# Kernel tuning notes

Hardware: AMD Instinct MI355X
Metric: run time of the kernel (lower is better)

The kernel has to match this reference:

```python
import jax, jax.numpy as jnp
import numpy as np

# Model dims (match init_kwargs)
B, S, H = 1, 2048, 1024
E = 16            # n_routed_experts
I = 768           # moe_intermediate_size
TOPK = 4          # num_experts_per_tok
G = 4             # n_group
TOPK_G = 2        # topk_group
SCALE = 2.5       # routed_scaling_factor
N_SHARED = 1      # n_shared_experts


def setup_inputs() -> dict:
    key = jax.random.key(0)
    ks = jax.random.split(key, 9)
    def rn(k, shape, scale=0.02):
        return jax.random.normal(k, shape, dtype=jnp.float32) * scale
    return dict(
        hidden_states=jax.random.normal(ks[0], (B, S, H), dtype=jnp.float32),
        gate_w=rn(ks[1], (E, H)),
        gate_bias=jax.random.normal(ks[2], (E,), dtype=jnp.float32) * 0.1,
        w1=rn(ks[3], (E, I, H)),   # gate_proj weights [out,in]
        w2=rn(ks[4], (E, H, I)),   # down_proj weights
        w3=rn(ks[5], (E, I, H)),   # up_proj weights
        ws1=rn(ks[6], (I * N_SHARED, H)),
        ws2=rn(ks[7], (H, I * N_SHARED)),
        ws3=rn(ks[8], (I * N_SHARED, H)),
    )


def _route(x, gate_w, gate_bias):
    """noaux_tc routing: sigmoid scores + bias, group top-k, top_k experts."""
    n = x.shape[0]
    logits = jnp.einsum('nh,eh->ne', x.astype(jnp.float32), gate_w)  # [N,E]
    scores = jax.nn.sigmoid(logits)
    sb = scores + gate_bias                                          # biased scores
    # group score = sum of top-2 biased scores in each group
    gs = sb.reshape(n, G, E // G)
    group_scores = jnp.sum(jax.lax.top_k(gs, 2)[0], axis=-1)         # [N,G]
    _, gidx = jax.lax.top_k(group_scores, TOPK_G)                    # [N,TOPK_G]
    gmask = jnp.sum(jax.nn.one_hot(gidx, G, dtype=sb.dtype), axis=1) # [N,G]
    emask = jnp.repeat(gmask, E // G, axis=-1)                       # [N,E]
    masked = jnp.where(emask > 0, sb, -jnp.inf)
    _, tidx = jax.lax.top_k(masked, TOPK)                            # [N,TOPK]
    w = jnp.take_along_axis(scores, tidx, axis=1)                    # unbiased weights
    w = w / (jnp.sum(w, axis=-1, keepdims=True) + 1e-20)             # norm_topk_prob
    return tidx, w * SCALE


def reference(hidden_states, gate_w, gate_bias, w1, w2, w3, ws1, ws2, ws3):
    b, s, h = hidden_states.shape
    x = hidden_states.reshape(-1, h)                                 # [N,H]
    tidx, tw = _route(x, gate_w, gate_bias)
    n = x.shape[0]
    # dense combine weights [N,E] (zero for unselected experts)
    combine = jnp.zeros((n, E), x.dtype).at[jnp.arange(n)[:, None], tidx].add(tw)
    # grouped SwiGLU experts (dense-over-experts reference form)
    g = jnp.einsum('nh,eih->nei', x, w1)
    u = jnp.einsum('nh,eih->nei', x, w3)
    hact = jax.nn.silu(g) * u * combine[:, :, None]
    y = jnp.einsum('nei,ehi->nh', hact, w2)
    # shared expert SwiGLU
    shared = jnp.einsum('ni,hi->nh', jax.nn.silu(x @ ws1.T) * (x @ ws3.T), ws2)
    return (y + shared).reshape(b, s, h)
```

## Files before the change

### kernel.cpp

```cpp
#include <hip/hip_runtime.h>
#include <hip/hip_bf16.h>
#include <math.h>

#define N_TOK 2048
#define H_DIM 1024
#define N_EXP 16
#define I_DIM 768
#define TOPK 4
#define SCALE 2.5f
#define MAX_TILES 96

typedef __attribute__((ext_vector_type(8))) short bf16x8;
typedef __attribute__((ext_vector_type(4))) float f32x4;

#define OFF_COUNTS   0
#define OFF_OFFSETS  128
#define OFF_TILES    256
#define OFF_TOKIDS   768
#define OFF_TOKW     (OFF_TOKIDS + N_EXP*N_TOK*4)
#define OFF_XB       (OFF_TOKW + N_EXP*N_TOK*4)
#define OFF_HACT     (OFF_XB + (size_t)N_TOK*H_DIM*2)
#define OFF_WB1      (OFF_HACT + (size_t)N_TOK*(TOPK+1)*I_DIM*2)
#define OFF_WB2      (OFF_WB1 + (size_t)N_EXP*I_DIM*H_DIM*2)
#define OFF_WB3      (OFF_WB2 + (size_t)N_EXP*H_DIM*I_DIM*2)
#define OFF_WSB1     (OFF_WB3 + (size_t)N_EXP*I_DIM*H_DIM*2)
#define OFF_WSB2     (OFF_WSB1 + (size_t)I_DIM*H_DIM*2)
#define OFF_WSB3     (OFF_WSB2 + (size_t)H_DIM*I_DIM*2)
#define OFF_GWT      (OFF_WSB3 + (size_t)I_DIM*H_DIM*2)

__device__ __forceinline__ ushort f2bf(float f) {
    union { __hip_bfloat16 h; ushort u; } cv;
    cv.h = __float2bfloat16(f);
    return cv.u;
}
__device__ __forceinline__ unsigned pack2(float lo, float hi) {
    return (unsigned)f2bf(lo) | ((unsigned)f2bf(hi) << 16);
}
__device__ __forceinline__ void async_copy16(const void* g, void* l) {
    __builtin_amdgcn_global_load_lds(
        (const __attribute__((address_space(1))) unsigned int*)g,
        (__attribute__((address_space(3))) unsigned int*)l, 16, 0, 0);
}

struct WcArgs {
    const float* src[7];
    ushort* dst[7];
    int n4[7];
};
__global__ void k_wconv(WcArgs a) {
    int id = blockIdx.y;
    const float4* s = (const float4*)a.src[id];
    uint2* d = (uint2*)a.dst[id];
    int n4 = a.n4[id];
    int stride = gridDim.x * 256;
    for (int i = blockIdx.x * 256 + threadIdx.x; i < n4; i += stride) {
        float4 v = s[i];
        uint2 p;
        p.x = pack2(v.x, v.y);
        p.y = pack2(v.z, v.w);
        d[i] = p;
    }
}

__global__ void k_gwt(const float* __restrict__ gw, float* __restrict__ gwT) {
    int i = blockIdx.x * 256 + threadIdx.x;
    int k = i >> 4, e = i & 15;
    gwT[i] = gw[e * H_DIM + k];
}

__launch_bounds__(256)
__global__ void k_route(const float* __restrict__ x, const float* __restrict__ gwT,
                        const float* __restrict__ gb,
                        int* __restrict__ counts, int* __restrict__ tok_ids,
                        float* __restrict__ tok_w) {
    __shared__ float lgs[4][N_EXP + 1];
    int tid = threadIdx.x;
    int wv = tid >> 6, lane = tid & 63;
    int e = lane & 15, ks = lane >> 4;
    int n = blockIdx.x * 4 + wv;

    const float* xr = x + (size_t)n * H_DIM + ks * 256;
    const float* wr = gwT + ks * 256 * N_EXP + e;
    float a0 = 0.f, a1 = 0.f, a2 = 0.f, a3 = 0.f;
#pragma unroll 8
    for (int k = 0; k < 256; k += 4) {
        float4 xv = *(const float4*)(xr + k);
        a0 += xv.x * wr[(k + 0) * N_EXP];
        a1 += xv.y * wr[(k + 1) * N_EXP];
        a2 += xv.z * wr[(k + 2) * N_EXP];
        a3 += xv.w * wr[(k + 3) * N_EXP];
    }
    float acc = (a0 + a1) + (a2 + a3);
    acc += __shfl_xor(acc, 16);
    acc += __shfl_xor(acc, 32);
    if (lane < 16) lgs[wv][lane] = acc;
    __syncthreads();

    if (tid < 4) {
        int n2 = blockIdx.x * 4 + tid;
        float sc[N_EXP], sb[N_EXP];
        for (int ee = 0; ee < N_EXP; ee++) {
            float l = lgs[tid][ee];
            sc[ee] = 1.f / (1.f + expf(-l));
            sb[ee] = sc[ee] + gb[ee];
        }
        float gsc[4];
        for (int g = 0; g < 4; g++) {
            float m1 = -1e30f, m2 = -1e30f;
            for (int j = 0; j < 4; j++) {
                float v = sb[4 * g + j];
                if (v > m1) { m2 = m1; m1 = v; }
                else if (v > m2) m2 = v;
            }
            gsc[g] = m1 + m2;
        }
        int g1 = 0;
        for (int g = 1; g < 4; g++) if (gsc[g] > gsc[g1]) g1 = g;
        int g2 = -1;
        for (int g = 0; g < 4; g++) {
            if (g == g1) continue;
            if (g2 < 0 || gsc[g] > gsc[g2]) g2 = g;
        }
        bool allowed[N_EXP];
        for (int ee = 0; ee < N_EXP; ee++) {
            int grp = ee >> 2;
            allowed[ee] = (grp == g1) || (grp == g2);
        }
        int chosen[TOPK];
        float wsum = 0.f;
        for (int k = 0; k < TOPK; k++) {
            int best = -1;
            for (int ee = 0; ee < N_EXP; ee++) {
                if (!allowed[ee]) continue;
                if (best < 0 || sb[ee] > sb[best]) best = ee;
            }
            chosen[k] = best;
            allowed[best] = false;
            wsum += sc[best];
        }
        float inv = SCALE / (wsum + 1e-20f);
        for (int k = 0; k < TOPK; k++) {
            int ee = chosen[k];
            int p = atomicAdd(&counts[ee], 1);
            tok_ids[ee * N_TOK + p] = n2;
            tok_w[ee * N_TOK + p] = sc[ee] * inv;
        }
    }
}

__global__ void k_scan(const int* __restrict__ counts, int* __restrict__ offsets,
                       int* __restrict__ tiles) {
    if (threadIdx.x == 0 && blockIdx.x == 0) {
        int off = 0;
        for (int e = 0; e < N_EXP; e++) { offsets[e] = off; off += counts[e]; }
        offsets[N_EXP] = off;
        int t = 0;
        for (int e = 0; e < N_EXP; e++)
            for (int m0 = 0; m0 < counts[e]; m0 += 128)
                tiles[t++] = e | ((m0 >> 7) << 5);
        for (int m0 = 0; m0 < N_TOK; m0 += 128)
            tiles[t++] = N_EXP | ((m0 >> 7) << 5);
        for (; t < MAX_TILES; t++) tiles[t] = -1;
    }
}

__launch_bounds__(256, 4)
__global__ void k_gateup(const ushort* __restrict__ xb, const ushort* __restrict__ wb1,
                         const ushort* __restrict__ wb3, const ushort* __restrict__ wsb1,
                         const ushort* __restrict__ wsb3, const int* __restrict__ counts,
                         const int* __restrict__ offsets, const int* __restrict__ tiles,
                         const int* __restrict__ tok_ids, const float* __restrict__ tok_w,
                         ushort* __restrict__ hact) {
    int desc = tiles[blockIdx.x];
    if (desc < 0) return;
    int e = desc & 31;
    int m0 = (desc >> 5) * 128;
    int i0 = blockIdx.y * 64;
    int Me = (e == N_EXP) ? N_TOK : counts[e];
    const ushort* W1 = (e == N_EXP) ? wsb1 : wb1 + (size_t)e * I_DIM * H_DIM;
    const ushort* W3 = (e == N_EXP) ? wsb3 : wb3 + (size_t)e * I_DIM * H_DIM;
    int base = offsets[e];

    __shared__ ushort As[128][64];
    __shared__ ushort Bs[128][64];
    __shared__ float tws[128];

    int tid = threadIdx.x;
    int wv = tid >> 6, lane = tid & 63;
    int seg = lane & 7, rsub = lane >> 3;
    int gch = (seg ^ rsub) * 8;

    if (tid < 128) {
        int r = m0 + tid;
        tws[tid] = (e == N_EXP) ? 1.f : ((r < Me) ? tok_w[e * N_TOK + r] : 0.f);
    }

    const ushort* aptr[4];
#pragma unroll
    for (int j = 0; j < 4; j++) {
        int gr = m0 + wv * 32 + j * 8 + rsub;
        int tok = (e == N_EXP) ? gr : ((gr < Me) ? tok_ids[e * N_TOK + gr] : 0);
        aptr[j] = xb + (size_t)tok * H_DIM + gch;
    }
    const ushort* bptr[4];
#pragma unroll
    for (int j = 0; j < 4; j++) {
        int r = wv * 32 + j * 8 + rsub;
        const ushort* W = (r < 64) ? (W1 + (size_t)(i0 + r) * H_DIM)
                                   : (W3 + (size_t)(i0 + r - 64) * H_DIM);
        bptr[j] = W + gch;
    }

    int quad = lane >> 4, lr = lane & 15, rx = lr & 7;
    f32x4 acc[2][8] = {};

    const int NK = H_DIM / 64;
    for (int k = 0; k < NK; k++) {
        int off = k * 64;
#pragma unroll
        for (int j = 0; j < 4; j++) async_copy16(aptr[j] + off, &As[wv * 32 + j * 8][0]);
#pragma unroll
        for (int j = 0; j < 4; j++) async_copy16(bptr[j] + off, &Bs[wv * 32 + j * 8][0]);
        __syncthreads();
#pragma unroll
        for (int ks = 0; ks < 2; ks++) {
            int co = ((ks * 4 + quad) ^ rx) * 8;
            bf16x8 a0 = *(const bf16x8*)&As[wv * 32 + lr][co];
            bf16x8 a1 = *(const bf16x8*)&As[wv * 32 + 16 + lr][co];
#pragma unroll
            for (int ni = 0; ni < 8; ni++) {
                bf16x8 bf = *(const bf16x8*)&Bs[ni * 16 + lr][co];
                acc[0][ni] = __builtin_amdgcn_mfma_f32_16x16x32_bf16(a0, bf, acc[0][ni], 0, 0, 0);
                acc[1][ni] = __builtin_amdgcn_mfma_f32_16x16x32_bf16(a1, bf, acc[1][ni], 0, 0, 0);
            }
        }
        __syncthreads();
    }

#pragma unroll
    for (int mi = 0; mi < 2; mi++) {
#pragma unroll
        for (int ni = 0; ni < 4; ni++) {
            f32x4 g = acc[mi][ni];
            f32x4 u = acc[mi][ni + 4];
#pragma unroll
            for (int rg = 0; rg < 4; rg++) {
                int ml = wv * 32 + mi * 16 + quad * 4 + rg;
                int row = m0 + ml;
                if (row < Me) {
                    float gg = g[rg], uu = u[rg];
                    float act = (gg / (1.f + expf(-gg))) * uu * tws[ml];
                    hact[(size_t)(base + row) * I_DIM + i0 + ni * 16 + lr] = f2bf(act);
                }
            }
        }
    }
}

__launch_bounds__(256, 4)
__global__ void k_down(const ushort* __restrict__ hact, const ushort* __restrict__ wb2,
                       const ushort* __restrict__ wsb2, const int* __restrict__ counts,
                       const int* __restrict__ offsets, const int* __restrict__ tiles,
                       const int* __restrict__ tok_ids, float* __restrict__ out) {
    int desc = tiles[blockIdx.x];
    if (desc < 0) return;
    int e = desc & 31;
    int m0 = (desc >> 5) * 128;
    int h0 = blockIdx.y * 128;
    int Me = (e == N_EXP) ? N_TOK : counts[e];
    const ushort* W2 = (e == N_EXP) ? wsb2 : wb2 + (size_t)e * H_DIM * I_DIM;
    int base = offsets[e];

    __shared__ ushort As[128][64];
    __shared__ ushort Bs[128][64];
    __shared__ int toks[128];

    int tid = threadIdx.x;
    int wv = tid >> 6, lane = tid & 63;
    int seg = lane & 7, rsub = lane >> 3;
    int gch = (seg ^ rsub) * 8;

    if (tid < 128) {
        int r = m0 + tid;
        toks[tid] = (e == N_EXP) ? r : ((r < Me) ? tok_ids[e * N_TOK + r] : 0);
    }

    const ushort* aptr[4];
#pragma unroll
    for (int j = 0; j < 4; j++) {
        int row = wv * 32 + j * 8 + rsub;
        aptr[j] = hact + (size_t)(base + m0 + row) * I_DIM + gch;
    }
    const ushort* bptr[4];
#pragma unroll
    for (int j = 0; j < 4; j++) {
        int r = wv * 32 + j * 8 + rsub;
        bptr[j] = W2 + (size_t)(h0 + r) * I_DIM + gch;
    }

    int quad = lane >> 4, lr = lane & 15, rx = lr & 7;
    f32x4 acc[2][8] = {};

    const int NK = I_DIM / 64;
    for (int k = 0; k < NK; k++) {
        int off = k * 64;
#pragma unroll
        for (int j = 0; j < 4; j++) async_copy16(aptr[j] + off, &As[wv * 32 + j * 8][0]);
#pragma unroll
        for (int j = 0; j < 4; j++) async_copy16(bptr[j] + off, &Bs[wv * 32 + j * 8][0]);
        __syncthreads();
#pragma unroll
        for (int ks = 0; ks < 2; ks++) {
            int co = ((ks * 4 + quad) ^ rx) * 8;
            bf16x8 a0 = *(const bf16x8*)&As[wv * 32 + lr][co];
            bf16x8 a1 = *(const bf16x8*)&As[wv * 32 + 16 + lr][co];
#pragma unroll
            for (int ni = 0; ni < 8; ni++) {
                bf16x8 bf = *(const bf16x8*)&Bs[ni * 16 + lr][co];
                acc[0][ni] = __builtin_amdgcn_mfma_f32_16x16x32_bf16(a0, bf, acc[0][ni], 0, 0, 0);
                acc[1][ni] = __builtin_amdgcn_mfma_f32_16x16x32_bf16(a1, bf, acc[1][ni], 0, 0, 0);
            }
        }
        __syncthreads();
    }

#pragma unroll
    for (int mi = 0; mi < 2; mi++) {
#pragma unroll
        for (int ni = 0; ni < 8; ni++) {
#pragma unroll
            for (int rg = 0; rg < 4; rg++) {
                int ml = wv * 32 + mi * 16 + quad * 4 + rg;
                int row = m0 + ml;
                if (row < Me) {
                    int tok = toks[ml];
                    atomicAdd(&out[(size_t)tok * H_DIM + h0 + ni * 16 + lr],
                              acc[mi][ni][rg]);
                }
            }
        }
    }
}

extern "C" void kernel_launch(void* const* d_in, const int* in_sizes, int n_in,
                              void* d_out, int out_size, void* d_ws, size_t ws_size,
                              hipStream_t stream) {
    const float* x   = (const float*)d_in[0];
    const float* gw  = (const float*)d_in[1];
    const float* gb  = (const float*)d_in[2];
    const float* w1  = (const float*)d_in[3];
    const float* w2  = (const float*)d_in[4];
    const float* w3  = (const float*)d_in[5];
    const float* ws1 = (const float*)d_in[6];
    const float* ws2 = (const float*)d_in[7];
    const float* ws3 = (const float*)d_in[8];
    float* out = (float*)d_out;

    char* wsb = (char*)d_ws;
    int* counts   = (int*)(wsb + OFF_COUNTS);
    int* offsets  = (int*)(wsb + OFF_OFFSETS);
    int* tiles    = (int*)(wsb + OFF_TILES);
    int* tok_ids  = (int*)(wsb + OFF_TOKIDS);
    float* tok_w  = (float*)(wsb + OFF_TOKW);
    ushort* xb    = (ushort*)(wsb + OFF_XB);
    ushort* hact  = (ushort*)(wsb + OFF_HACT);
    ushort* wb1   = (ushort*)(wsb + OFF_WB1);
    ushort* wb2   = (ushort*)(wsb + OFF_WB2);
    ushort* wb3   = (ushort*)(wsb + OFF_WB3);
    ushort* wsb1  = (ushort*)(wsb + OFF_WSB1);
    ushort* wsb2  = (ushort*)(wsb + OFF_WSB2);
    ushort* wsb3  = (ushort*)(wsb + OFF_WSB3);
    float* gwT    = (float*)(wsb + OFF_GWT);

    hipMemsetAsync(wsb, 0, 128, stream);
    hipMemsetAsync(d_out, 0, (size_t)out_size * 4, stream);

    WcArgs wa;
    wa.src[0] = w1;  wa.dst[0] = wb1;  wa.n4[0] = N_EXP * I_DIM * H_DIM / 4;
    wa.src[1] = w2;  wa.dst[1] = wb2;  wa.n4[1] = N_EXP * H_DIM * I_DIM / 4;
    wa.src[2] = w3;  wa.dst[2] = wb3;  wa.n4[2] = N_EXP * I_DIM * H_DIM / 4;
    wa.src[3] = ws1; wa.dst[3] = wsb1; wa.n4[3] = I_DIM * H_DIM / 4;
    wa.src[4] = ws2; wa.dst[4] = wsb2; wa.n4[4] = H_DIM * I_DIM / 4;
    wa.src[5] = ws3; wa.dst[5] = wsb3; wa.n4[5] = I_DIM * H_DIM / 4;
    wa.src[6] = x;   wa.dst[6] = xb;   wa.n4[6] = N_TOK * H_DIM / 4;
    k_wconv<<<dim3(3072, 7), 256, 0, stream>>>(wa);

    k_gwt<<<N_EXP * H_DIM / 256, 256, 0, stream>>>(gw, gwT);
    k_route<<<N_TOK / 4, 256, 0, stream>>>(x, gwT, gb, counts, tok_ids, tok_w);
    k_scan<<<1, 1, 0, stream>>>(counts, offsets, tiles);
    {
        dim3 grid(MAX_TILES, I_DIM / 64);
        k_gateup<<<grid, 256, 0, stream>>>(xb, wb1, wb3, wsb1, wsb3, counts, offsets,
                                           tiles, tok_ids, tok_w, hact);
    }
    {
        dim3 grid(MAX_TILES, H_DIM / 128);
        k_down<<<grid, 256, 0, stream>>>(hact, wb2, wsb2, counts, offsets, tiles,
                                         tok_ids, out);
    }
}
```

Measured before the change: 363.5 us.

## Fuse fp32-to-bf16 weight conversion into expert GEMM tile loads

Removes the separate pass that converted all expert and shared weights to bf16. The gate/up and down GEMM kernels now read fp32 weights directly, register-prefetch the next K slice, and pack to bf16 while storing into the swizzled LDS tile. Only the activations get a small dedicated conversion kernel. This avoids a full read and write of every weight each call, but the GEMMs now fetch twice as many bytes per weight tile, once for each token tile, and do the B staging through registers rather than async LDS copies.

```diff
diff --git a/kernel.cpp b/kernel.cpp
--- a/kernel.cpp
+++ b/kernel.cpp
@@ -20,13 +20,7 @@
 #define OFF_TOKW     (OFF_TOKIDS + N_EXP*N_TOK*4)
 #define OFF_XB       (OFF_TOKW + N_EXP*N_TOK*4)
 #define OFF_HACT     (OFF_XB + (size_t)N_TOK*H_DIM*2)
-#define OFF_WB1      (OFF_HACT + (size_t)N_TOK*(TOPK+1)*I_DIM*2)
-#define OFF_WB2      (OFF_WB1 + (size_t)N_EXP*I_DIM*H_DIM*2)
-#define OFF_WB3      (OFF_WB2 + (size_t)N_EXP*H_DIM*I_DIM*2)
-#define OFF_WSB1     (OFF_WB3 + (size_t)N_EXP*I_DIM*H_DIM*2)
-#define OFF_WSB2     (OFF_WSB1 + (size_t)I_DIM*H_DIM*2)
-#define OFF_WSB3     (OFF_WSB2 + (size_t)H_DIM*I_DIM*2)
-#define OFF_GWT      (OFF_WSB3 + (size_t)I_DIM*H_DIM*2)
+#define OFF_GWT      (OFF_HACT + (size_t)N_TOK*(TOPK+1)*I_DIM*2)
 
 __device__ __forceinline__ ushort f2bf(float f) {
     union { __hip_bfloat16 h; ushort u; } cv;
@@ -41,25 +35,18 @@
         (const __attribute__((address_space(1))) unsigned int*)g,
         (__attribute__((address_space(3))) unsigned int*)l, 16, 0, 0);
 }
-
-struct WcArgs {
-    const float* src[7];
-    ushort* dst[7];
-    int n4[7];
-};
-__global__ void k_wconv(WcArgs a) {
-    int id = blockIdx.y;
-    const float4* s = (const float4*)a.src[id];
-    uint2* d = (uint2*)a.dst[id];
-    int n4 = a.n4[id];
-    int stride = gridDim.x * 256;
-    for (int i = blockIdx.x * 256 + threadIdx.x; i < n4; i += stride) {
-        float4 v = s[i];
-        uint2 p;
-        p.x = pack2(v.x, v.y);
-        p.y = pack2(v.z, v.w);
-        d[i] = p;
-    }
+__device__ __forceinline__ uint4 pack8(float4 a, float4 b) {
+    uint4 p;
+    p.x = pack2(a.x, a.y); p.y = pack2(a.z, a.w);
+    p.z = pack2(b.x, b.y); p.w = pack2(b.z, b.w);
+    return p;
+}
+
+__global__ void k_xconv(const float* __restrict__ x, ushort* __restrict__ xb) {
+    int idx = (blockIdx.x * 256 + threadIdx.x) * 8;
+    float4 a = *(const float4*)(x + idx);
+    float4 b = *(const float4*)(x + idx + 4);
+    *(uint4*)(xb + idx) = pack8(a, b);
 }
 
 __global__ void k_gwt(const float* __restrict__ gw, float* __restrict__ gwT) {
@@ -165,9 +152,9 @@
 }
 
 __launch_bounds__(256, 4)
-__global__ void k_gateup(const ushort* __restrict__ xb, const ushort* __restrict__ wb1,
-                         const ushort* __restrict__ wb3, const ushort* __restrict__ wsb1,
-                         const ushort* __restrict__ wsb3, const int* __restrict__ counts,
+__global__ void k_gateup(const ushort* __restrict__ xb, const float* __restrict__ w1,
+                         const float* __restrict__ w3, const float* __restrict__ ws1,
+                         const float* __restrict__ ws3, const int* __restrict__ counts,
                          const int* __restrict__ offsets, const int* __restrict__ tiles,
                          const int* __restrict__ tok_ids, const float* __restrict__ tok_w,
                          ushort* __restrict__ hact) {
@@ -177,8 +164,8 @@
     int m0 = (desc >> 5) * 128;
     int i0 = blockIdx.y * 64;
     int Me = (e == N_EXP) ? N_TOK : counts[e];
-    const ushort* W1 = (e == N_EXP) ? wsb1 : wb1 + (size_t)e * I_DIM * H_DIM;
-    const ushort* W3 = (e == N_EXP) ? wsb3 : wb3 + (size_t)e * I_DIM * H_DIM;
+    const float* W1 = (e == N_EXP) ? ws1 : w1 + (size_t)e * I_DIM * H_DIM;
+    const float* W3 = (e == N_EXP) ? ws3 : w3 + (size_t)e * I_DIM * H_DIM;
     int base = offsets[e];
 
     __shared__ ushort As[128][64];
@@ -202,26 +189,42 @@
         int tok = (e == N_EXP) ? gr : ((gr < Me) ? tok_ids[e * N_TOK + gr] : 0);
         aptr[j] = xb + (size_t)tok * H_DIM + gch;
     }
-    const ushort* bptr[4];
+    const float* bptr[4];
 #pragma unroll
     for (int j = 0; j < 4; j++) {
         int r = wv * 32 + j * 8 + rsub;
-        const ushort* W = (r < 64) ? (W1 + (size_t)(i0 + r) * H_DIM)
-                                   : (W3 + (size_t)(i0 + r - 64) * H_DIM);
+        const float* W = (r < 64) ? (W1 + (size_t)(i0 + r) * H_DIM)
+                                  : (W3 + (size_t)(i0 + r - 64) * H_DIM);
         bptr[j] = W + gch;
     }
 
     int quad = lane >> 4, lr = lane & 15, rx = lr & 7;
     f32x4 acc[2][8] = {};
+    float4 bv[4][2];
+
+#pragma unroll
+    for (int j = 0; j < 4; j++) {
+        bv[j][0] = *(const float4*)(bptr[j]);
+        bv[j][1] = *(const float4*)(bptr[j] + 4);
+    }
 
     const int NK = H_DIM / 64;
     for (int k = 0; k < NK; k++) {
         int off = k * 64;
 #pragma unroll
+        for (int j = 0; j < 4; j++)
+            *(uint4*)&Bs[wv * 32 + j * 8 + rsub][seg * 8] = pack8(bv[j][0], bv[j][1]);
+#pragma unroll
         for (int j = 0; j < 4; j++) async_copy16(aptr[j] + off, &As[wv * 32 + j * 8][0]);
-#pragma unroll
-        for (int j = 0; j < 4; j++) async_copy16(bptr[j] + off, &Bs[wv * 32 + j * 8][0]);
         __syncthreads();
+        if (k + 1 < NK) {
+            int o2 = off + 64;
+#pragma unroll
+            for (int j = 0; j < 4; j++) {
+                bv[j][0] = *(const float4*)(bptr[j] + o2);
+                bv[j][1] = *(const float4*)(bptr[j] + o2 + 4);
+            }
+        }
 #pragma unroll
         for (int ks = 0; ks < 2; ks++) {
             int co = ((ks * 4 + quad) ^ rx) * 8;
@@ -258,8 +261,8 @@
 }
 
 __launch_bounds__(256, 4)
-__global__ void k_down(const ushort* __restrict__ hact, const ushort* __restrict__ wb2,
-                       const ushort* __restrict__ wsb2, const int* __restrict__ counts,
+__global__ void k_down(const ushort* __restrict__ hact, const float* __restrict__ w2,
+                       const float* __restrict__ ws2, const int* __restrict__ counts,
                        const int* __restrict__ offsets, const int* __restrict__ tiles,
                        const int* __restrict__ tok_ids, float* __restrict__ out) {
     int desc = tiles[blockIdx.x];
@@ -268,7 +271,7 @@
     int m0 = (desc >> 5) * 128;
     int h0 = blockIdx.y * 128;
     int Me = (e == N_EXP) ? N_TOK : counts[e];
-    const ushort* W2 = (e == N_EXP) ? wsb2 : wb2 + (size_t)e * H_DIM * I_DIM;
+    const float* W2 = (e == N_EXP) ? ws2 : w2 + (size_t)e * H_DIM * I_DIM;
     int base = offsets[e];
 
     __shared__ ushort As[128][64];
@@ -291,7 +294,7 @@
         int row = wv * 32 + j * 8 + rsub;
         aptr[j] = hact + (size_t)(base + m0 + row) * I_DIM + gch;
     }
-    const ushort* bptr[4];
+    const float* bptr[4];
 #pragma unroll
     for (int j = 0; j < 4; j++) {
         int r = wv * 32 + j * 8 + rsub;
@@ -300,15 +303,31 @@
 
     int quad = lane >> 4, lr = lane & 15, rx = lr & 7;
     f32x4 acc[2][8] = {};
+    float4 bv[4][2];
+
+#pragma unroll
+    for (int j = 0; j < 4; j++) {
+        bv[j][0] = *(const float4*)(bptr[j]);
+        bv[j][1] = *(const float4*)(bptr[j] + 4);
+    }
 
     const int NK = I_DIM / 64;
     for (int k = 0; k < NK; k++) {
         int off = k * 64;
 #pragma unroll
+        for (int j = 0; j < 4; j++)
+            *(uint4*)&Bs[wv * 32 + j * 8 + rsub][seg * 8] = pack8(bv[j][0], bv[j][1]);
+#pragma unroll
         for (int j = 0; j < 4; j++) async_copy16(aptr[j] + off, &As[wv * 32 + j * 8][0]);
-#pragma unroll
-        for (int j = 0; j < 4; j++) async_copy16(bptr[j] + off, &Bs[wv * 32 + j * 8][0]);
         __syncthreads();
+        if (k + 1 < NK) {
+            int o2 = off + 64;
+#pragma unroll
+            for (int j = 0; j < 4; j++) {
+                bv[j][0] = *(const float4*)(bptr[j] + o2);
+                bv[j][1] = *(const float4*)(bptr[j] + o2 + 4);
+            }
+        }
 #pragma unroll
         for (int ks = 0; ks < 2; ks++) {
             int co = ((ks * 4 + quad) ^ rx) * 8;
@@ -364,38 +383,23 @@
     float* tok_w  = (float*)(wsb + OFF_TOKW);
     ushort* xb    = (ushort*)(wsb + OFF_XB);
     ushort* hact  = (ushort*)(wsb + OFF_HACT);
-    ushort* wb1   = (ushort*)(wsb + OFF_WB1);
-    ushort* wb2   = (ushort*)(wsb + OFF_WB2);
-    ushort* wb3   = (ushort*)(wsb + OFF_WB3);
-    ushort* wsb1  = (ushort*)(wsb + OFF_WSB1);
-    ushort* wsb2  = (ushort*)(wsb + OFF_WSB2);
-    ushort* wsb3  = (ushort*)(wsb + OFF_WSB3);
     float* gwT    = (float*)(wsb + OFF_GWT);
 
     hipMemsetAsync(wsb, 0, 128, stream);
     hipMemsetAsync(d_out, 0, (size_t)out_size * 4, stream);
 
-    WcArgs wa;
-    wa.src[0] = w1;  wa.dst[0] = wb1;  wa.n4[0] = N_EXP * I_DIM * H_DIM / 4;
-    wa.src[1] = w2;  wa.dst[1] = wb2;  wa.n4[1] = N_EXP * H_DIM * I_DIM / 4;
-    wa.src[2] = w3;  wa.dst[2] = wb3;  wa.n4[2] = N_EXP * I_DIM * H_DIM / 4;
-    wa.src[3] = ws1; wa.dst[3] = wsb1; wa.n4[3] = I_DIM * H_DIM / 4;
-    wa.src[4] = ws2; wa.dst[4] = wsb2; wa.n4[4] = H_DIM * I_DIM / 4;
-    wa.src[5] = ws3; wa.dst[5] = wsb3; wa.n4[5] = I_DIM * H_DIM / 4;
-    wa.src[6] = x;   wa.dst[6] = xb;   wa.n4[6] = N_TOK * H_DIM / 4;
-    k_wconv<<<dim3(3072, 7), 256, 0, stream>>>(wa);
-
+    k_xconv<<<N_TOK * H_DIM / (256 * 8), 256, 0, stream>>>(x, xb);
     k_gwt<<<N_EXP * H_DIM / 256, 256, 0, stream>>>(gw, gwT);
     k_route<<<N_TOK / 4, 256, 0, stream>>>(x, gwT, gb, counts, tok_ids, tok_w);
     k_scan<<<1, 1, 0, stream>>>(counts, offsets, tiles);
     {
         dim3 grid(MAX_TILES, I_DIM / 64);
-        k_gateup<<<grid, 256, 0, stream>>>(xb, wb1, wb3, wsb1, wsb3, counts, offsets,
+        k_gateup<<<grid, 256, 0, stream>>>(xb, w1, w3, ws1, ws3, counts, offsets,
                                            tiles, tok_ids, tok_w, hact);
     }
     {
         dim3 grid(MAX_TILES, H_DIM / 128);
-        k_down<<<grid, 256, 0, stream>>>(hact, wb2, wsb2, counts, offsets, tiles,
+        k_down<<<grid, 256, 0, stream>>>(hact, w2, ws2, counts, offsets, tiles,
                                          tok_ids, out);
     }
 }
```

After: 379.3 us. 1.04x slower.
